# Kernel tuning notes

Measured on AMD Instinct MI355X. Metric: run time of the kernel, lower is better.

Reference implementation:

```python
import jax, jax.numpy as jnp
import numpy as np

D_MODEL = 1024
NUM_HEADS = 16
HEAD_DIM = D_MODEL // NUM_HEADS


def setup_inputs() -> dict:
    key = jax.random.key(0)
    ks = jax.random.split(key, 5)
    x = jax.random.normal(ks[0], (2, 2048, D_MODEL), dtype=jnp.float32)
    s = 1.0 / np.sqrt(D_MODEL)
    # nn.Linear weight is [out, in]; y = x @ W.T
    Wq = jax.random.normal(ks[1], (D_MODEL, D_MODEL), dtype=jnp.float32) * s
    Wk = jax.random.normal(ks[2], (D_MODEL, D_MODEL), dtype=jnp.float32) * s
    Wv = jax.random.normal(ks[3], (D_MODEL, D_MODEL), dtype=jnp.float32) * s
    Wo = jax.random.normal(ks[4], (D_MODEL, D_MODEL), dtype=jnp.float32) * s
    return {"x": x, "Wq": Wq, "Wk": Wk, "Wv": Wv, "Wo": Wo}


def reference(x, Wq, Wk, Wv, Wo):
    b, s, d = x.shape
    h, hd = NUM_HEADS, HEAD_DIM
    # projections (Linear: x @ W.T), reshape to [b, h, s, hd]
    def proj(W):
        return (x @ W.T).reshape(b, s, h, hd).transpose(0, 2, 1, 3)
    Q, K, V = proj(Wq), proj(Wk), proj(Wv)
    # NOTE: original scales by 1/sqrt(d_model), not 1/sqrt(head_dim)
    scores = jnp.einsum('bhqd,bhkd->bhqk', Q, K) / jnp.sqrt(jnp.float32(d))
    attn = jax.nn.softmax(scores, axis=-1)
    ctx = jnp.einsum('bhqk,bhkd->bhqd', attn, V)
    ctx = ctx.transpose(0, 2, 1, 3).reshape(b, s, d)
    return ctx @ Wo.T
```

## Files before the change

### kernel.cpp

```cpp
#include <hip/hip_runtime.h>
#include <cstddef>
#include <cstdint>

#define SEQ 2048
#define DM 1024
#define NH 16
#define HD 64

typedef _Float16 f16;
typedef __attribute__((ext_vector_type(8))) _Float16 f16x8;
typedef __attribute__((ext_vector_type(4))) _Float16 f16x4;
typedef __attribute__((ext_vector_type(2))) _Float16 f16x2;
typedef __attribute__((ext_vector_type(4))) float f32x4;

__global__ __launch_bounds__(256) void cast_all(const float* __restrict__ x,
                                                const float* __restrict__ Wq,
                                                const float* __restrict__ Wk,
                                                const float* __restrict__ Wv,
                                                const float* __restrict__ Wo,
                                                f16* __restrict__ dst) {
  const int i = blockIdx.x * 256 + threadIdx.x;
  const float* src;
  int off;
  if (i < 1048576) {
    src = x; off = i;
  } else {
    const int j = i - 1048576;
    const int wsel = j >> 18;
    src = (wsel == 0) ? Wq : (wsel == 1) ? Wk : (wsel == 2) ? Wv : Wo;
    off = j & 262143;
  }
  const float4 v = ((const float4*)src)[off];
  f16x4 o = {(f16)v.x, (f16)v.y, (f16)v.z, (f16)v.w};
  ((f16x4*)dst)[i] = o;
}

__device__ __forceinline__ void gload16(const void* g, void* lds) {
  __builtin_amdgcn_global_load_lds((const __attribute__((address_space(1))) void*)g,
                                   (__attribute__((address_space(3))) void*)lds,
                                   16, 0, 0);
}

__device__ __forceinline__ void gemm_tile(const f16* __restrict__ A,
                                          const f16* __restrict__ B,
                                          f16* As, f16* Bs,
                                          int K, f32x4 acc[4][4]) {
  const int t = threadIdx.x;
  const int lane = t & 63;
  const int w = t >> 6;
  const int wm = (w & 1) << 6, wn = (w >> 1) << 6;
  const int srow = lane >> 2, scol = lane & 3;
  const int fr = lane & 15, q = lane >> 4;
  for (int k0 = 0; k0 < K; k0 += 32) {
    __syncthreads();
#pragma unroll
    for (int c = 0; c < 2; ++c) {
      const int chunk = (w << 1) + c;
      const int row = (chunk << 4) + srow;
      gload16(A + (size_t)row * K + k0 + (scol << 3), As + (chunk << 9));
      gload16(B + (size_t)row * K + k0 + (scol << 3), Bs + (chunk << 9));
    }
    __syncthreads();
    f16x8 af[4], bfr[4];
#pragma unroll
    for (int i = 0; i < 4; ++i)
      af[i] = *(const f16x8*)(As + (wm + (i << 4) + fr) * 32 + (q << 3));
#pragma unroll
    for (int j = 0; j < 4; ++j)
      bfr[j] = *(const f16x8*)(Bs + (wn + (j << 4) + fr) * 32 + (q << 3));
#pragma unroll
    for (int i = 0; i < 4; ++i)
#pragma unroll
      for (int j = 0; j < 4; ++j)
        acc[i][j] = __builtin_amdgcn_mfma_f32_16x16x32_f16(af[i], bfr[j],
                                                           acc[i][j], 0, 0, 0);
  }
}

#define QSCALE 0.04508422003f
__global__ __launch_bounds__(256) void gemm_qkv(
    const f16* __restrict__ xb, const f16* __restrict__ Wqb,
    const f16* __restrict__ Wkb, const f16* __restrict__ Wvb,
    f16* __restrict__ Qb, f16* __restrict__ Kb, f16* __restrict__ Vtg) {
  __shared__ f16 smem[16384];
  f16* As = smem;
  f16* Bs = smem + 4096;
  const int which = blockIdx.x >> 3;
  const int bn = (blockIdx.x & 7) << 7;
  const int bm = blockIdx.y << 7;
  const f16* B = (which == 0) ? Wqb : (which == 1) ? Wkb : Wvb;
  f32x4 acc[4][4] = {};
  gemm_tile(xb + (size_t)bm * DM, B + (size_t)bn * DM, As, Bs, DM, acc);
  const int lane = threadIdx.x & 63, w = threadIdx.x >> 6;
  const int wm = (w & 1) << 6, wn = (w >> 1) << 6;
  const int col = lane & 15, q = lane >> 4;
  if (which < 2) {
    f16* C = (which == 0) ? Qb : Kb;
    const float sc = (which == 0) ? QSCALE : 1.0f;
#pragma unroll
    for (int i = 0; i < 4; ++i) {
      const int m = bm + wm + (i << 4) + (q << 2);
#pragma unroll
      for (int j = 0; j < 4; ++j) {
        const int n = bn + wn + (j << 4) + col;
#pragma unroll
        for (int r = 0; r < 4; ++r)
          C[(size_t)(m + r) * DM + n] = (f16)(acc[i][j][r] * sc);
      }
    }
  } else {
    __syncthreads();
#pragma unroll
    for (int i = 0; i < 4; ++i) {
      const int m0 = wm + (i << 4) + (q << 2);
      const int cm = m0 >> 3, sub = (m0 >> 2) & 1;
#pragma unroll
      for (int j = 0; j < 4; ++j) {
        const int nl = wn + (j << 4) + col;
        f16x4 o = {(f16)acc[i][j][0], (f16)acc[i][j][1],
                   (f16)acc[i][j][2], (f16)acc[i][j][3]};
        *(f16x4*)(smem + nl * 128 +
                  ((cm ^ (nl & 15) ^ ((nl >> 4) & 3)) << 3) + (sub << 2)) = o;
      }
    }
    __syncthreads();
    const int b = bm >> 11, sb = bm & 2047;
    const int d = threadIdx.x & 63;
#pragma unroll
    for (int step = 0; step < 16; ++step) {
      const int idx = (threadIdx.x >> 6) + (step << 2);
      const int hh = idx >> 5, s4 = idx & 31;
      const int nl = (hh << 6) + d;
      const int cm = s4 >> 1, sub = s4 & 1;
      const f16x4 v = *(const f16x4*)(smem + nl * 128 +
                                      ((cm ^ (nl & 15) ^ ((nl >> 4) & 3)) << 3) +
                                      (sub << 2));
      const int bh = (b << 4) + (bn >> 6) + hh;
      const int sg = sb + (s4 << 2);
      const size_t flat = ((size_t)bh << 17) + ((size_t)(sg >> 6) << 12) +
                          ((size_t)(d >> 4) << 10) + (((size_t)(s4 >> 3) & 1) << 9) +
                          (((size_t)s4 & 3) << 7) + (((size_t)d & 15) << 3) +
                          (((size_t)(s4 >> 2) & 1) << 2);
      *(f16x4*)(Vtg + flat) = v;
    }
  }
}

__global__ __launch_bounds__(256) void gemm_out(const f16* __restrict__ Ab,
                                                const f16* __restrict__ Wob,
                                                float* __restrict__ out) {
  __shared__ f16 As[128 * 32];
  __shared__ f16 Bs[128 * 32];
  const int bn = blockIdx.x << 7, bm = blockIdx.y << 7;
  f32x4 acc[4][4] = {};
  gemm_tile(Ab + (size_t)bm * DM, Wob + (size_t)bn * DM, As, Bs, DM, acc);
  const int lane = threadIdx.x & 63, w = threadIdx.x >> 6;
  const int wm = (w & 1) << 6, wn = (w >> 1) << 6;
  const int col = lane & 15, q = lane >> 4;
#pragma unroll
  for (int i = 0; i < 4; ++i) {
    const int m = bm + wm + (i << 4) + (q << 2);
#pragma unroll
    for (int j = 0; j < 4; ++j) {
      const int n = bn + wn + (j << 4) + col;
#pragma unroll
      for (int r = 0; r < 4; ++r)
        out[(size_t)(m + r) * DM + n] = acc[i][j][r];
    }
  }
}

__global__ __launch_bounds__(256, 2) void attn_mfma(const f16* __restrict__ Qb,
                                                    const f16* __restrict__ Kb,
                                                    const f16* __restrict__ Vtg,
                                                    f16* __restrict__ Ctx) {
  __shared__ f16 smem[16384];
  const int t = threadIdx.x, lane = t & 63, w = t >> 6;
  const int fr = lane & 15, quad = lane >> 4;
  const int i = blockIdx.x;
  const int j = i >> 3;
  const int bh = ((i & 7) << 2) + (j >> 4);
  const int qt16 = j & 15;
  const int b = bh >> 4, h = bh & 15;

  const size_t qrow0 = (size_t)b * SEQ + qt16 * 128 + w * 32;

  f16x8 Qf[2][2];
#pragma unroll
  for (int qt = 0; qt < 2; ++qt)
#pragma unroll
    for (int hf = 0; hf < 2; ++hf)
      Qf[qt][hf] = *(const f16x8*)(Qb + (qrow0 + qt * 16 + fr) * DM + h * HD +
                                   hf * 32 + (quad << 3));

  const int krow = lane >> 2;
  const int kkc = ((lane & 3) - (lane >> 3)) & 3;
  const f16* Kg = Kb + ((size_t)b * SEQ + 16 * w + krow) * DM + h * HD + (kkc << 3);
  const f16* Vg = Vtg + ((size_t)bh << 17) + (((w << 7) + lane) << 3);

  const int crd = ((fr >> 1) << 3) | ((fr & 1) << 2) | (((fr >> 1) + quad) & 3);

  f16* K0 = smem;
  f16* K1 = smem + 4096;
  f16* V0 = smem + 8192;
  f16* V1 = smem + 12288;

  auto stage = [&](int kt, f16* Kimg, f16* Vimg) {
#pragma unroll
    for (int hf = 0; hf < 2; ++hf)
      gload16(Kg + (size_t)kt * 64 * DM + hf * 32,
              Kimg + (hf << 11) + (w << 9));
#pragma unroll
    for (int c = 0; c < 2; ++c)
      gload16(Vg + kt * 4096 + (c << 9), Vimg + (w << 10) + (c << 9));
  };

  f32x4 acc[2][4] = {};
  float lacc[2] = {0.f, 0.f};

  stage(0, K0, V0);

  auto body = [&](int kt, f16* KR, f16* VR, f16* KW, f16* VW) {
    __syncthreads();
    if (kt < 31) stage(kt + 1, KW, VW);

    f16x8 Kf[4][2];
#pragma unroll
    for (int mt = 0; mt < 4; ++mt)
#pragma unroll
      for (int hf = 0; hf < 2; ++hf)
        Kf[mt][hf] = *(const f16x8*)(KR + (crd << 3) + (hf << 11) + (mt << 9));
    f16x8 Vf[4][2];
#pragma unroll
    for (int dt = 0; dt < 4; ++dt)
#pragma unroll
      for (int kp = 0; kp < 2; ++kp)
        Vf[dt][kp] = *(const f16x8*)(VR + (((dt << 1) | kp) << 9) +
                                     (quad << 7) + (fr << 3));

    f32x4 z[2][4] = {};
#pragma unroll
    for (int hf = 0; hf < 2; ++hf)
#pragma unroll
      for (int qt = 0; qt < 2; ++qt)
#pragma unroll
        for (int mt = 0; mt < 4; ++mt)
          z[qt][mt] = __builtin_amdgcn_mfma_f32_16x16x32_f16(Kf[mt][hf], Qf[qt][hf],
                                                             z[qt][mt], 0, 0, 0);

    f16x4 pf[2][4];
#pragma unroll
    for (int qt = 0; qt < 2; ++qt)
#pragma unroll
      for (int mt = 0; mt < 4; ++mt) {
        const float p0 = __builtin_amdgcn_exp2f(z[qt][mt][0]);
        const float p1 = __builtin_amdgcn_exp2f(z[qt][mt][1]);
        const float p2 = __builtin_amdgcn_exp2f(z[qt][mt][2]);
        const float p3 = __builtin_amdgcn_exp2f(z[qt][mt][3]);
        lacc[qt] += (p0 + p1) + (p2 + p3);
        const f16x2 lo = __builtin_bit_cast(f16x2, __builtin_amdgcn_cvt_pkrtz(p0, p1));
        const f16x2 hi = __builtin_bit_cast(f16x2, __builtin_amdgcn_cvt_pkrtz(p2, p3));
        f16x4 pv; pv.x = lo.x; pv.y = lo.y; pv.z = hi.x; pv.w = hi.y;
        pf[qt][mt] = pv;
      }

#pragma unroll
    for (int kc = 0; kc < 4; ++kc)
#pragma unroll
      for (int dt = 0; dt < 4; ++dt) {
        const f16x8 v8 = Vf[dt][kc >> 1];
        const f16x4 vh = (kc & 1) ? __builtin_shufflevector(v8, v8, 4, 5, 6, 7)
                                  : __builtin_shufflevector(v8, v8, 0, 1, 2, 3);
#pragma unroll
        for (int qt = 0; qt < 2; ++qt)
          acc[qt][dt] = __builtin_amdgcn_mfma_f32_16x16x16f16(vh, pf[qt][kc],
                                                              acc[qt][dt], 0, 0, 0);
      }
  };

  for (int kt = 0; kt < 32; kt += 2) {
    body(kt, K0, V0, K1, V1);
    body(kt + 1, K1, V1, K0, V0);
  }

  float inv[2];
#pragma unroll
  for (int qt = 0; qt < 2; ++qt) {
    float l = lacc[qt];
    l += __shfl_xor(l, 16);
    l += __shfl_xor(l, 32);
    inv[qt] = __builtin_amdgcn_rcpf(l);
  }

  __syncthreads();
  f16* T = smem + (w << 11);
#pragma unroll
  for (int qt = 0; qt < 2; ++qt)
#pragma unroll
    for (int dt = 0; dt < 4; ++dt) {
      f16x4 o = {(f16)(acc[qt][dt][0] * inv[qt]), (f16)(acc[qt][dt][1] * inv[qt]),
                 (f16)(acc[qt][dt][2] * inv[qt]), (f16)(acc[qt][dt][3] * inv[qt])};
      *(f16x4*)(T + (qt * 16 + fr) * 64 + dt * 16 + (quad << 2)) = o;
    }
#pragma unroll
  for (int p = 0; p < 4; ++p) {
    const int ql = p * 8 + (lane >> 3);
    const f16x8 v = *(const f16x8*)(T + ql * 64 + ((lane & 7) << 3));
    *(f16x8*)(Ctx + (qrow0 + ql) * DM + h * HD + ((lane & 7) << 3)) = v;
  }
}

extern "C" void kernel_launch(void* const* d_in, const int* in_sizes, int n_in,
                              void* d_out, int out_size, void* d_ws, size_t ws_size,
                              hipStream_t stream) {
  const float* x  = (const float*)d_in[0];
  const float* Wq = (const float*)d_in[1];
  const float* Wk = (const float*)d_in[2];
  const float* Wv = (const float*)d_in[3];
  const float* Wo = (const float*)d_in[4];

  char* ws = (char*)d_ws;
  f16* xb  = (f16*)(ws);
  f16* Wb  = (f16*)(ws + (8u << 20));
  f16* Wqb = Wb;
  f16* Wkb = Wb + 1048576;
  f16* Wvb = Wb + 2097152;
  f16* Wob = Wb + 3145728;
  f16* Qb  = (f16*)(ws + (16u << 20));
  f16* Kb  = (f16*)(ws + (24u << 20));
  f16* Vtg = (f16*)(ws + (32u << 20));
  f16* Ctx = (f16*)(ws + (40u << 20));

  cast_all<<<8192, 256, 0, stream>>>(x, Wq, Wk, Wv, Wo, xb);

  gemm_qkv<<<dim3(24, 32), 256, 0, stream>>>(xb, Wqb, Wkb, Wvb, Qb, Kb, Vtg);
  attn_mfma<<<dim3(2 * NH * (SEQ / 128)), 256, 0, stream>>>(Qb, Kb, Vtg, Ctx);
  gemm_out<<<dim3(8, 32), 256, 0, stream>>>(Ctx, Wob, (float*)d_out);
}
```

Baseline: 195.5 us.

## Widen GEMM k-step to 64 with XOR-swizzled LDS, retile out-proj, relayout V

The shared GEMM tile loop now stages 64-wide K slices instead of 32, using an XOR swizzle on LDS columns to avoid bank conflicts. This halves the number of barrier pairs per tile. The output projection is retiled to 128x64 blocks with 512 blocks, giving better CU occupancy on a 1024-wide output. The V-transpose layout written by the QKV kernel is changed so the attention kernel can load f16x4 V fragments directly without shuffling. The trade-off is more LDS per block and more index arithmetic.

```diff
diff --git a/kernel.cpp b/kernel.cpp
--- a/kernel.cpp
+++ b/kernel.cpp
@@ -49,31 +49,43 @@
   const int lane = t & 63;
   const int w = t >> 6;
   const int wm = (w & 1) << 6, wn = (w >> 1) << 6;
-  const int srow = lane >> 2, scol = lane & 3;
+  const int srow = lane >> 3, sg = lane & 7;
   const int fr = lane & 15, q = lane >> 4;
-  for (int k0 = 0; k0 < K; k0 += 32) {
-    __syncthreads();
-#pragma unroll
-    for (int c = 0; c < 2; ++c) {
-      const int chunk = (w << 1) + c;
-      const int row = (chunk << 4) + srow;
-      gload16(A + (size_t)row * K + k0 + (scol << 3), As + (chunk << 9));
-      gload16(B + (size_t)row * K + k0 + (scol << 3), Bs + (chunk << 9));
-    }
-    __syncthreads();
-    f16x8 af[4], bfr[4];
-#pragma unroll
-    for (int i = 0; i < 4; ++i)
-      af[i] = *(const f16x8*)(As + (wm + (i << 4) + fr) * 32 + (q << 3));
-#pragma unroll
-    for (int j = 0; j < 4; ++j)
-      bfr[j] = *(const f16x8*)(Bs + (wn + (j << 4) + fr) * 32 + (q << 3));
-#pragma unroll
-    for (int i = 0; i < 4; ++i)
-#pragma unroll
-      for (int j = 0; j < 4; ++j)
-        acc[i][j] = __builtin_amdgcn_mfma_f32_16x16x32_f16(af[i], bfr[j],
-                                                           acc[i][j], 0, 0, 0);
+  const int scol = (sg ^ srow) << 3;
+  for (int k0 = 0; k0 < K; k0 += 64) {
+    __syncthreads();
+#pragma unroll
+    for (int c = 0; c < 4; ++c) {
+      const int row = (w << 5) + (c << 3) + srow;
+      gload16(A + (size_t)row * K + k0 + scol, As + (w << 11) + (c << 9));
+      gload16(B + (size_t)row * K + k0 + scol, Bs + (w << 11) + (c << 9));
+    }
+    __syncthreads();
+    f16x8 af[4][2], bf[4][2];
+#pragma unroll
+    for (int i = 0; i < 4; ++i) {
+      const int row = wm + (i << 4) + fr;
+#pragma unroll
+      for (int kh = 0; kh < 2; ++kh)
+        af[i][kh] = *(const f16x8*)(As + row * 64 +
+                                    ((((kh << 2) | q) ^ (row & 7)) << 3));
+    }
+#pragma unroll
+    for (int j = 0; j < 4; ++j) {
+      const int row = wn + (j << 4) + fr;
+#pragma unroll
+      for (int kh = 0; kh < 2; ++kh)
+        bf[j][kh] = *(const f16x8*)(Bs + row * 64 +
+                                    ((((kh << 2) | q) ^ (row & 7)) << 3));
+    }
+#pragma unroll
+    for (int kh = 0; kh < 2; ++kh)
+#pragma unroll
+      for (int i = 0; i < 4; ++i)
+#pragma unroll
+        for (int j = 0; j < 4; ++j)
+          acc[i][j] = __builtin_amdgcn_mfma_f32_16x16x32_f16(af[i][kh], bf[j][kh],
+                                                             acc[i][j], 0, 0, 0);
   }
 }
 
@@ -84,7 +96,7 @@
     f16* __restrict__ Qb, f16* __restrict__ Kb, f16* __restrict__ Vtg) {
   __shared__ f16 smem[16384];
   f16* As = smem;
-  f16* Bs = smem + 4096;
+  f16* Bs = smem + 8192;
   const int which = blockIdx.x >> 3;
   const int bn = (blockIdx.x & 7) << 7;
   const int bm = blockIdx.y << 7;
@@ -138,9 +150,8 @@
       const int bh = (b << 4) + (bn >> 6) + hh;
       const int sg = sb + (s4 << 2);
       const size_t flat = ((size_t)bh << 17) + ((size_t)(sg >> 6) << 12) +
-                          ((size_t)(d >> 4) << 10) + (((size_t)(s4 >> 3) & 1) << 9) +
-                          (((size_t)s4 & 3) << 7) + (((size_t)d & 15) << 3) +
-                          (((size_t)(s4 >> 2) & 1) << 2);
+                          (((size_t)(s4 >> 2) & 3) << 10) +
+                          (((size_t)s4 & 3) << 8) + ((size_t)d << 2);
       *(f16x4*)(Vtg + flat) = v;
     }
   }
@@ -149,20 +160,63 @@
 __global__ __launch_bounds__(256) void gemm_out(const f16* __restrict__ Ab,
                                                 const f16* __restrict__ Wob,
                                                 float* __restrict__ out) {
-  __shared__ f16 As[128 * 32];
-  __shared__ f16 Bs[128 * 32];
-  const int bn = blockIdx.x << 7, bm = blockIdx.y << 7;
-  f32x4 acc[4][4] = {};
-  gemm_tile(Ab + (size_t)bm * DM, Wob + (size_t)bn * DM, As, Bs, DM, acc);
-  const int lane = threadIdx.x & 63, w = threadIdx.x >> 6;
-  const int wm = (w & 1) << 6, wn = (w >> 1) << 6;
-  const int col = lane & 15, q = lane >> 4;
-#pragma unroll
-  for (int i = 0; i < 4; ++i) {
+  __shared__ f16 As[128 * 64];
+  __shared__ f16 Bs[64 * 64];
+  const int bn = blockIdx.x << 6, bm = blockIdx.y << 7;
+  const int t = threadIdx.x, lane = t & 63, w = t >> 6;
+  const int srow = lane >> 3, sg = lane & 7;
+  const int fr = lane & 15, q = lane >> 4;
+  const int scol = (sg ^ srow) << 3;
+  const f16* A = Ab + (size_t)bm * DM;
+  const f16* B = Wob + (size_t)bn * DM;
+  const int wm = w << 5;
+  f32x4 acc[2][4] = {};
+  for (int k0 = 0; k0 < DM; k0 += 64) {
+    __syncthreads();
+#pragma unroll
+    for (int c = 0; c < 4; ++c) {
+      const int row = (w << 5) + (c << 3) + srow;
+      gload16(A + (size_t)row * DM + k0 + scol, As + (w << 11) + (c << 9));
+    }
+#pragma unroll
+    for (int c = 0; c < 2; ++c) {
+      const int row = (w << 4) + (c << 3) + srow;
+      gload16(B + (size_t)row * DM + k0 + scol, Bs + (w << 10) + (c << 9));
+    }
+    __syncthreads();
+    f16x8 af[2][2], bf[4][2];
+#pragma unroll
+    for (int i = 0; i < 2; ++i) {
+      const int row = wm + (i << 4) + fr;
+#pragma unroll
+      for (int kh = 0; kh < 2; ++kh)
+        af[i][kh] = *(const f16x8*)(As + row * 64 +
+                                    ((((kh << 2) | q) ^ (row & 7)) << 3));
+    }
+#pragma unroll
+    for (int j = 0; j < 4; ++j) {
+      const int row = (j << 4) + fr;
+#pragma unroll
+      for (int kh = 0; kh < 2; ++kh)
+        bf[j][kh] = *(const f16x8*)(Bs + row * 64 +
+                                    ((((kh << 2) | q) ^ (row & 7)) << 3));
+    }
+#pragma unroll
+    for (int kh = 0; kh < 2; ++kh)
+#pragma unroll
+      for (int i = 0; i < 2; ++i)
+#pragma unroll
+        for (int j = 0; j < 4; ++j)
+          acc[i][j] = __builtin_amdgcn_mfma_f32_16x16x32_f16(af[i][kh], bf[j][kh],
+                                                             acc[i][j], 0, 0, 0);
+  }
+  const int col = lane & 15;
+#pragma unroll
+  for (int i = 0; i < 2; ++i) {
     const int m = bm + wm + (i << 4) + (q << 2);
 #pragma unroll
     for (int j = 0; j < 4; ++j) {
-      const int n = bn + wn + (j << 4) + col;
+      const int n = bn + (j << 4) + col;
 #pragma unroll
       for (int r = 0; r < 4; ++r)
         out[(size_t)(m + r) * DM + n] = acc[i][j][r];
@@ -230,13 +284,13 @@
 #pragma unroll
       for (int hf = 0; hf < 2; ++hf)
         Kf[mt][hf] = *(const f16x8*)(KR + (crd << 3) + (hf << 11) + (mt << 9));
-    f16x8 Vf[4][2];
+    f16x4 Vf[4][4];
 #pragma unroll
     for (int dt = 0; dt < 4; ++dt)
 #pragma unroll
-      for (int kp = 0; kp < 2; ++kp)
-        Vf[dt][kp] = *(const f16x8*)(VR + (((dt << 1) | kp) << 9) +
-                                     (quad << 7) + (fr << 3));
+      for (int kc = 0; kc < 4; ++kc)
+        Vf[dt][kc] = *(const f16x4*)(VR + (kc << 10) + (quad << 8) +
+                                     (((dt << 4) | fr) << 2));
 
     f32x4 z[2][4] = {};
 #pragma unroll
@@ -267,15 +321,11 @@
 #pragma unroll
     for (int kc = 0; kc < 4; ++kc)
 #pragma unroll
-      for (int dt = 0; dt < 4; ++dt) {
-        const f16x8 v8 = Vf[dt][kc >> 1];
-        const f16x4 vh = (kc & 1) ? __builtin_shufflevector(v8, v8, 4, 5, 6, 7)
-                                  : __builtin_shufflevector(v8, v8, 0, 1, 2, 3);
+      for (int dt = 0; dt < 4; ++dt)
 #pragma unroll
         for (int qt = 0; qt < 2; ++qt)
-          acc[qt][dt] = __builtin_amdgcn_mfma_f32_16x16x16f16(vh, pf[qt][kc],
+          acc[qt][dt] = __builtin_amdgcn_mfma_f32_16x16x16f16(Vf[dt][kc], pf[qt][kc],
                                                               acc[qt][dt], 0, 0, 0);
-      }
   };
 
   for (int kt = 0; kt < 32; kt += 2) {
@@ -335,5 +385,5 @@
 
   gemm_qkv<<<dim3(24, 32), 256, 0, stream>>>(xb, Wqb, Wkb, Wvb, Qb, Kb, Vtg);
   attn_mfma<<<dim3(2 * NH * (SEQ / 128)), 256, 0, stream>>>(Qb, Kb, Vtg, Ctx);
-  gemm_out<<<dim3(8, 32), 256, 0, stream>>>(Ctx, Wob, (float*)d_out);
-}
+  gemm_out<<<dim3(16, 32), 256, 0, stream>>>(Ctx, Wob, (float*)d_out);
+}
```

Result: faster. 182.1 us (-6.8%).
